# Kernel tuning notes

Hardware: AMD Instinct MI355X
Metric: run time of the kernel (lower is better)

Reference implementation:

```python
import jax, jax.numpy as jnp
import numpy as np

# Sizes: batch, mapper input dim, subspace dim n, ambient dim k (= n, no equalities),
# number of linear inequalities, number of quadratic constraints.
B, IN_DIM, N, K, M_LIN, QC = 32768, 256, 128, 128, 1024, 16


def setup_inputs() -> dict:
    rng = np.random.default_rng(0)
    x = rng.standard_normal((B, IN_DIM, 1), dtype=np.float32)
    # mapper = nn.Linear(IN_DIM, N)
    W = (rng.standard_normal((N, IN_DIM)) / np.sqrt(IN_DIM)).astype(np.float32)
    b = (0.01 * rng.standard_normal((N,))).astype(np.float32)
    # Linear inequalities A_p z <= b_p, strictly feasible at z0 = 0
    z0 = np.zeros((N, 1), dtype=np.float32)
    A_p = rng.standard_normal((M_LIN, N)).astype(np.float32)
    b_p = (A_p @ z0 + rng.uniform(0.5, 1.5, (M_LIN, 1))).astype(np.float32)
    D = (A_p / (b_p - A_p @ z0)).astype(np.float32)  # D = A_p / ((b_p - A_p z0) 1^T)
    # No equality constraints: y = NA_E z + yp with NA_E = I, yp = 0, y0 = z0
    NA_E = np.eye(K, N, dtype=np.float32)
    yp = np.zeros((K, 1), dtype=np.float32)
    y0 = NA_E @ z0 + yp
    # Quadratic constraints 0.5 y'P y + q'y + r <= 0, strictly feasible at y0.
    # Precompute phi, delta exactly as in ConstraintModule.__init__ (RAYEN branch).
    all_phi = np.empty((QC, 1, K), dtype=np.float32)
    all_delta = np.empty((QC, K, K), dtype=np.float32)
    for i in range(QC):
        G = (rng.standard_normal((K, K)) / np.sqrt(K)).astype(np.float32)
        P = G.T @ G + 0.1 * np.eye(K, dtype=np.float32)
        q = (0.1 * rng.standard_normal((K, 1))).astype(np.float32)
        val0 = 0.5 * y0.T @ P @ y0 + q.T @ y0
        r = -(val0 + np.float32(rng.uniform(0.5, 2.0)))  # value at y0 strictly negative
        quad_at_y0 = 0.5 * y0.T @ P @ y0 + q.T @ y0 + r   # [1,1], < 0
        sigma = 2.0 * quad_at_y0                           # scalar < 0
        g = y0.T @ P + q.T                                 # [1,K]
        all_phi[i] = -g / sigma
        all_delta[i] = (g.T @ g - 4.0 * quad_at_y0 * 0.5 * P) / np.square(sigma)
    return {
        "x": jnp.asarray(x),
        "W": jnp.asarray(W),
        "b": jnp.asarray(b),
        "D": jnp.asarray(D),
        "NA_E": jnp.asarray(NA_E),
        "yp": jnp.asarray(yp),
        "z0": jnp.asarray(z0),
        "all_phi": jnp.asarray(all_phi),
        "all_delta": jnp.asarray(all_delta),
    }


def reference(x, W, b, D, NA_E, yp, z0, all_phi, all_delta):
    Bn = x.shape[0]
    # mapper: x.view(B,-1) -> Linear -> unsqueeze(2)
    v = (x.reshape(Bn, -1) @ W.T + b)[:, :, None]                     # [B,n,1]
    norm_v = jnp.sqrt(jnp.sum(v * v, axis=(1, 2), keepdims=True))    # [B,1,1]
    v_bar = v / jnp.maximum(norm_v, 1e-12)                           # F.normalize
    # kappa from linear constraints: relu(max_m (D v_bar)_m)
    Dv = jnp.einsum('mn,bno->bmo', D, v_bar)                         # [B,M,1]
    kappa = jax.nn.relu(jnp.max(Dv, axis=1, keepdims=True))          # [B,1,1]
    # kappa from quadratic constraints: phi_i rho + sqrt(rho' delta_i rho)
    rho = jnp.einsum('kn,bno->bko', NA_E, v_bar)[..., 0]             # [B,k]
    lin_term = rho @ all_phi[:, 0, :].T                              # [B,Q]
    dr = jnp.einsum('qkl,bl->bqk', all_delta, rho)                   # [B,Q,k]
    quad_term = jnp.einsum('bqk,bk->bq', dr, rho)                    # [B,Q]
    kappa_q = lin_term + jnp.sqrt(quad_term)                         # [B,Q]
    kappa_nl = jnp.max(kappa_q, axis=1)[:, None, None]               # [B,1,1]
    kappa = jnp.maximum(kappa, kappa_nl)
    # alpha = min(1/kappa, ||v||); z = z0 + alpha * v_bar; y = NA_E z + yp
    alpha = jnp.minimum(1.0 / kappa, norm_v)
    z = z0 + alpha * v_bar                                           # [B,n,1]
    y = jnp.einsum('kn,bno->bko', NA_E, z) + yp                      # [B,k,1]
    return y
```

## Files before the change

### kernel.cpp

```cpp
#include <hip/hip_runtime.h>
#include <hip/hip_bf16.h>


typedef __attribute__((ext_vector_type(8))) short short8;
typedef __attribute__((ext_vector_type(4))) float f32x4;

__device__ __forceinline__ float bf2f(unsigned short u) {
    union { unsigned int i; float f; } v; v.i = ((unsigned int)u) << 16; return v.f;
}
__device__ __forceinline__ unsigned short f2bf(float f) {
    union { float f; unsigned int i; } v; v.f = f;
    unsigned int r = v.i + 0x7FFFu + ((v.i >> 16) & 1u);
    return (unsigned short)(r >> 16);
}

template<int DT>
__device__ __forceinline__ short8 ld8(const void* p, size_t i) {
    if constexpr (DT == 1) {
        return *reinterpret_cast<const short8*>(reinterpret_cast<const unsigned short*>(p) + i);
    } else {
        const float* f = reinterpret_cast<const float*>(p) + i;
        short8 r;
#pragma unroll
        for (int j = 0; j < 8; ++j) r[j] = (short)f2bf(f[j]);
        return r;
    }
}
template<int DT>
__device__ __forceinline__ float ldf(const void* p, int i) {
    if constexpr (DT == 1) return bf2f(reinterpret_cast<const unsigned short*>(p)[i]);
    else return reinterpret_cast<const float*>(p)[i];
}

__device__ __forceinline__ void glds16(const void* g, void* l) {
    __builtin_amdgcn_global_load_lds(
        (const __attribute__((address_space(1))) void*)g,
        (__attribute__((address_space(3))) void*)l, 16, 0, 0);
}

__global__ void detect_dtype(const unsigned short* __restrict__ x, int* __restrict__ flag) {
    __shared__ int cnt;
    if (threadIdx.x == 0) cnt = 0;
    __syncthreads();
    float a = fabsf(bf2f(x[threadIdx.x]));
    int ok = (a > 1e-3f && a < 1e2f) ? 1 : 0;
    atomicAdd(&cnt, ok);
    __syncthreads();
    if (threadIdx.x == 0) *flag = (cnt > 200) ? 1 : 0;
}

template<int DT, int MODE>
__device__ __forceinline__ void rayen_body(
    const void* xp, const void* Wp, const void* bp, const void* Dp,
    const void* ypp, const void* z0p, const void* phip, const void* dltp,
    void* outp, const int* flag)
{
    if (*flag != DT) return;

    __shared__ unsigned char lds_big[49152];
    __shared__ unsigned char lds_rho[16384];
    __shared__ float lds_nsq[64][4];
    __shared__ float lds_dmax[64][4];
    __shared__ float lds_quad[64][16];
    __shared__ float lds_lin[64][16];
    __shared__ float lds_alpha[64];

    const int tid = threadIdx.x;
    const int lane = tid & 63;
    const int w = tid >> 6;
    const int hi = lane >> 4;
    const int lo = lane & 15;
    const size_t row0 = (size_t)blockIdx.x * 64;

    const unsigned char* Xb = (const unsigned char*)xp;
    const unsigned char* Db = (const unsigned char*)Dp;
    const unsigned char* Qb = (const unsigned char*)dltp;

#pragma unroll
    for (int i = 0; i < 8; ++i) {
        int ch = i * 256 + tid;
        int row = ((ch >> 9) << 4) | (ch & 15);
        int off = (((ch >> 6) & 7) << 6) | (((ch >> 4) & 3) << 4);
        if constexpr (DT == 1)
            glds16(Xb + (row0 + row) * 512 + off, lds_big + ch * 16);
        else {
            short8 v = ld8<0>(Xb, (row0 + row) * 256 + (off >> 1));
            *reinterpret_cast<short8*>(lds_big + ch * 16) = v;
        }
    }

    short8 wf[2][8];
#pragma unroll
    for (int ct = 0; ct < 2; ++ct)
#pragma unroll
        for (int kb = 0; kb < 8; ++kb)
            wf[ct][kb] = ld8<DT>(Wp, (size_t)(w * 32 + ct * 16 + lo) * 256 + kb * 32 + hi * 8);

    asm volatile("s_waitcnt vmcnt(0)" ::: "memory");
    __syncthreads();

    f32x4 acc1[2][4];
#pragma unroll
    for (int c = 0; c < 2; ++c)
#pragma unroll
        for (int r = 0; r < 4; ++r)
#pragma unroll
            for (int e = 0; e < 4; ++e) acc1[c][r][e] = 0.f;

#pragma unroll
    for (int kb = 0; kb < 8; ++kb) {
        short8 af[4];
#pragma unroll
        for (int rt = 0; rt < 4; ++rt)
            af[rt] = *reinterpret_cast<const short8*>(
                lds_big + (((rt << 3) | kb) << 10) + lane * 16);
#pragma unroll
        for (int ct = 0; ct < 2; ++ct)
#pragma unroll
            for (int rt = 0; rt < 4; ++rt)
                acc1[ct][rt] = __builtin_amdgcn_mfma_f32_16x16x32_bf16(af[rt], wf[ct][kb], acc1[ct][rt], 0, 0, 0);
    }

    float bv[2];
#pragma unroll
    for (int ct = 0; ct < 2; ++ct) bv[ct] = ldf<DT>(bp, w * 32 + ct * 16 + lo);
#pragma unroll
    for (int rt = 0; rt < 4; ++rt)
#pragma unroll
        for (int reg = 0; reg < 4; ++reg) {
            float s = 0.f;
#pragma unroll
            for (int ct = 0; ct < 2; ++ct) {
                float v = acc1[ct][rt][reg] + bv[ct];
                acc1[ct][rt][reg] = v;
                s += v * v;
            }
            s += __shfl_xor(s, 1);
            s += __shfl_xor(s, 2);
            s += __shfl_xor(s, 4);
            s += __shfl_xor(s, 8);
            if (lo == 0) lds_nsq[rt * 16 + hi * 4 + reg][w] = s;
        }
    __syncthreads();

#pragma unroll
    for (int rt = 0; rt < 4; ++rt)
#pragma unroll
        for (int reg = 0; reg < 4; ++reg) {
            int row = rt * 16 + hi * 4 + reg;
            float nsq = lds_nsq[row][0] + lds_nsq[row][1] + lds_nsq[row][2] + lds_nsq[row][3];
            float rinv = 1.0f / fmaxf(sqrtf(nsq), 1e-12f);
#pragma unroll
            for (int ct = 0; ct < 2; ++ct) {
                int col = w * 32 + ct * 16 + lo;
                unsigned short u = f2bf(acc1[ct][rt][reg] * rinv);
                *reinterpret_cast<unsigned short*>(
                    lds_rho + row * 256 + ((col * 2) ^ ((row & 7) << 4))) = u;
            }
        }
    __syncthreads();

    short8 af2[4][4];
#pragma unroll
    for (int rt = 0; rt < 4; ++rt)
#pragma unroll
        for (int kb = 0; kb < 4; ++kb) {
            int row = rt * 16 + lo;
            af2[rt][kb] = *reinterpret_cast<const short8*>(
                lds_rho + row * 256 + (((kb << 6) | (hi << 4)) ^ ((lo & 7) << 4)));
        }

    unsigned char* wbase = lds_big + w * 12288;
    auto stage_q = [&](int p, int b) {
        unsigned char* dst0 = wbase + b * 4096;
#pragma unroll
        for (int kb = 0; kb < 4; ++kb) {
            size_t grow;
            const void* base;
            if (p < 16) { base = Dp;   grow = (size_t)(p * 64 + w * 16 + lo); }
            else {
                int pd = p - 16;
                base = dltp;
                grow = (size_t)((((pd >> 3) * 4 + w) * 128) + ((pd & 7) * 16 + lo));
            }
            if constexpr (DT == 1)
                glds16((const unsigned char*)base + grow * 256 + kb * 64 + hi * 16,
                       dst0 + kb * 1024);
            else {
                short8 v = ld8<0>(base, grow * 128 + kb * 32 + hi * 8);
                *reinterpret_cast<short8*>(dst0 + kb * 1024 + lane * 16) = v;
            }
        }
    };

    f32x4 dmax[4];
#pragma unroll
    for (int rt = 0; rt < 4; ++rt)
#pragma unroll
        for (int e = 0; e < 4; ++e) dmax[rt][e] = -3e38f;
    f32x4 qsum[4];
#pragma unroll
    for (int rt = 0; rt < 4; ++rt)
#pragma unroll
        for (int e = 0; e < 4; ++e) qsum[rt][e] = 0.f;

    if constexpr (MODE != 1) {
        stage_q(0, 0);
        stage_q(1, 1);
#pragma unroll 1
        for (int p = 0; p < 48; ++p) {
            if constexpr (DT == 1) {
                if (p < 47) { asm volatile("s_waitcnt vmcnt(4)" ::: "memory"); }
                else        { asm volatile("s_waitcnt vmcnt(0)" ::: "memory"); }
            } else {
                asm volatile("s_waitcnt vmcnt(0) lgkmcnt(0)" ::: "memory");
            }
            __builtin_amdgcn_sched_barrier(0);
            if (p + 2 < 48) stage_q(p + 2, (p + 2) % 3);

            if constexpr (MODE != 2) {
                unsigned char* buf = wbase + (p % 3) * 4096;
                f32x4 acc[4];
#pragma unroll
                for (int rt = 0; rt < 4; ++rt)
#pragma unroll
                    for (int e = 0; e < 4; ++e) acc[rt][e] = 0.f;
#pragma unroll
                for (int kb = 0; kb < 4; ++kb) {
                    short8 bf = *reinterpret_cast<const short8*>(buf + kb * 1024 + lane * 16);
#pragma unroll
                    for (int rt = 0; rt < 4; ++rt)
                        acc[rt] = __builtin_amdgcn_mfma_f32_16x16x32_bf16(af2[rt][kb], bf, acc[rt], 0, 0, 0);
                }

                if (MODE == 3 || p < 16) {
#pragma unroll
                    for (int rt = 0; rt < 4; ++rt)
#pragma unroll
                        for (int e = 0; e < 4; ++e) dmax[rt][e] = fmaxf(dmax[rt][e], acc[rt][e]);
                } else {
                    int pd = p - 16;
                    int kr = (pd & 7) << 4;
#pragma unroll
                    for (int rt = 0; rt < 4; ++rt)
#pragma unroll
                        for (int e = 0; e < 4; ++e) {
                            int row = rt * 16 + hi * 4 + e;
                            float rvv = bf2f(*reinterpret_cast<const unsigned short*>(
                                lds_rho + row * 256 + ((((kr + lo) * 2)) ^ ((row & 7) << 4))));
                            qsum[rt][e] += acc[rt][e] * rvv;
                        }
                    if ((pd & 7) == 7) {
#pragma unroll
                        for (int rt = 0; rt < 4; ++rt)
#pragma unroll
                            for (int e = 0; e < 4; ++e) {
                                float s = qsum[rt][e];
                                s += __shfl_xor(s, 1);
                                s += __shfl_xor(s, 2);
                                s += __shfl_xor(s, 4);
                                s += __shfl_xor(s, 8);
                                if (lo == 0) lds_quad[rt * 16 + hi * 4 + e][((pd >> 3) << 2) | w] = s;
                                qsum[rt][e] = 0.f;
                            }
                    }
                }
            }
        }
    }

    if constexpr (MODE == 0 || MODE == 3) {
#pragma unroll
        for (int rt = 0; rt < 4; ++rt)
#pragma unroll
            for (int reg = 0; reg < 4; ++reg) {
                float m = dmax[rt][reg];
                m = fmaxf(m, __shfl_xor(m, 1));
                m = fmaxf(m, __shfl_xor(m, 2));
                m = fmaxf(m, __shfl_xor(m, 4));
                m = fmaxf(m, __shfl_xor(m, 8));
                if (lo == 0) lds_dmax[rt * 16 + hi * 4 + reg][w] = m;
            }
    }
    if constexpr (MODE == 1 || MODE == 2) {
        if (tid < 64) {
#pragma unroll
            for (int j = 0; j < 4; ++j) lds_dmax[tid][j] = 0.f;
        }
    }
    if constexpr (MODE != 0) {
        if (tid < 64) {
#pragma unroll
            for (int q = 0; q < 16; ++q) lds_quad[tid][q] = 0.f;
        }
    }

    if (w == 0) {
        f32x4 accp[4];
#pragma unroll
        for (int rt = 0; rt < 4; ++rt)
#pragma unroll
            for (int e = 0; e < 4; ++e) accp[rt][e] = 0.f;
#pragma unroll
        for (int kb = 0; kb < 4; ++kb) {
            short8 bp8 = ld8<DT>(phip, (size_t)lo * 128 + kb * 32 + hi * 8);
#pragma unroll
            for (int rt = 0; rt < 4; ++rt)
                accp[rt] = __builtin_amdgcn_mfma_f32_16x16x32_bf16(af2[rt][kb], bp8, accp[rt], 0, 0, 0);
        }
#pragma unroll
        for (int rt = 0; rt < 4; ++rt)
#pragma unroll
            for (int reg = 0; reg < 4; ++reg)
                lds_lin[rt * 16 + hi * 4 + reg][lo] = accp[rt][reg];
    }
    __syncthreads();

    if (tid < 64) {
        int row = tid;
        float nsq = lds_nsq[row][0] + lds_nsq[row][1] + lds_nsq[row][2] + lds_nsq[row][3];
        float norm = sqrtf(nsq);
        float kap = fmaxf(0.f, fmaxf(fmaxf(lds_dmax[row][0], lds_dmax[row][1]),
                                     fmaxf(lds_dmax[row][2], lds_dmax[row][3])));
#pragma unroll
        for (int q = 0; q < 16; ++q) {
            float kq = lds_lin[row][q] + sqrtf(fmaxf(lds_quad[row][q], 0.f));
            kap = fmaxf(kap, kq);
        }
        lds_alpha[row] = fminf(1.0f / kap, norm);
    }
    __syncthreads();

#pragma unroll
    for (int i = 0; i < 4; ++i) {
        int idx = tid + i * 256;
        int row = idx >> 4;
        int col0 = (idx & 15) * 8;
        float alpha = lds_alpha[row];
        short8 r8 = *reinterpret_cast<const short8*>(
            lds_rho + row * 256 + ((col0 * 2) ^ ((row & 7) << 4)));
        float yv[8];
#pragma unroll
        for (int j = 0; j < 8; ++j) {
            float vb = bf2f((unsigned short)r8[j]);
            yv[j] = ldf<DT>(z0p, col0 + j) + alpha * vb + ldf<DT>(ypp, col0 + j);
        }
        size_t obase = (row0 + row) * 128 + col0;
        if constexpr (DT == 1) {
            short8 pack;
#pragma unroll
            for (int j = 0; j < 8; ++j) pack[j] = (short)f2bf(yv[j]);
            *reinterpret_cast<short8*>(reinterpret_cast<unsigned short*>(outp) + obase) = pack;
        } else {
            f32x4 p0, p1;
#pragma unroll
            for (int j = 0; j < 4; ++j) { p0[j] = yv[j]; p1[j] = yv[4 + j]; }
            *reinterpret_cast<f32x4*>(reinterpret_cast<float*>(outp) + obase) = p0;
            *reinterpret_cast<f32x4*>(reinterpret_cast<float*>(outp) + obase + 4) = p1;
        }
    }
}

#define ARGS const void* xp, const void* Wp, const void* bp, const void* Dp, \
             const void* ypp, const void* z0p, const void* phip, const void* dltp, \
             void* outp, const int* flag
#define PASS xp, Wp, bp, Dp, ypp, z0p, phip, dltp, outp, flag

template<int DT>
__global__ __launch_bounds__(256, 2) void rayen_full(ARGS)      { rayen_body<DT, 0>(PASS); }
__global__ __launch_bounds__(256, 2) void rayen_abl_nopanel(ARGS)   { rayen_body<1, 1>(PASS); }
__global__ __launch_bounds__(256, 2) void rayen_abl_stageonly(ARGS) { rayen_body<1, 2>(PASS); }
__global__ __launch_bounds__(256, 2) void rayen_abl_mfmaonly(ARGS)  { rayen_body<1, 3>(PASS); }

extern "C" void kernel_launch(void* const* d_in, const int* in_sizes, int n_in,
                              void* d_out, int out_size, void* d_ws, size_t ws_size,
                              hipStream_t stream) {
    const void* x    = d_in[0];
    const void* W    = d_in[1];
    const void* b    = d_in[2];
    const void* D    = d_in[3];
    const void* yp   = d_in[5];
    const void* z0   = d_in[6];
    const void* phi  = d_in[7];
    const void* dlt  = d_in[8];
    int* flag = reinterpret_cast<int*>(d_ws);

    const int B = in_sizes[0] / 256;
    dim3 grid(B / 64), blk(256);

    detect_dtype<<<dim3(1), dim3(256), 0, stream>>>(
        reinterpret_cast<const unsigned short*>(x), flag);
    rayen_abl_nopanel<<<grid, blk, 0, stream>>>(x, W, b, D, yp, z0, phi, dlt, d_out, flag);
    rayen_abl_stageonly<<<grid, blk, 0, stream>>>(x, W, b, D, yp, z0, phi, dlt, d_out, flag);
    rayen_abl_mfmaonly<<<grid, blk, 0, stream>>>(x, W, b, D, yp, z0, phi, dlt, d_out, flag);
    rayen_full<1><<<grid, blk, 0, stream>>>(x, W, b, D, yp, z0, phi, dlt, d_out, flag);
    rayen_full<0><<<grid, blk, 0, stream>>>(x, W, b, D, yp, z0, phi, dlt, d_out, flag);
}
```

Baseline: 127.7 us.

## Split fused RAYEN kernel into staged kernels and drop ablation launches

Replaces the monolithic per-tile kernel with four kernels: a mapper GEMM that writes normalized v_bar and norms to workspace, a linear-constraint max kernel split over 4 M-groups, a quadratic-constraint kernel split over 16 constraints, and a small output kernel. It also stops launching the three ablation kernels that previously ran alongside the full kernel on every call. The goal is more blocks per stage for better occupancy, no serial 48-step panel loop per tile, and no redundant work. In exchange, v_bar makes an extra round trip through global memory, it re-stages from workspace, and more kernels are launched. It falls back to the fused kernel when the workspace is too small.

```diff
diff --git a/kernel.cpp b/kernel.cpp
--- a/kernel.cpp
+++ b/kernel.cpp
@@ -49,14 +49,340 @@
     if (threadIdx.x == 0) *flag = (cnt > 200) ? 1 : 0;
 }
 
-template<int DT, int MODE>
-__device__ __forceinline__ void rayen_body(
+template<int DT>
+__global__ __launch_bounds__(256, 2) void k1_vbar(
+    const void* __restrict__ xp, const void* __restrict__ Wp, const void* __restrict__ bp,
+    unsigned short* __restrict__ rho_g, float* __restrict__ norm_g,
+    const int* __restrict__ flag)
+{
+    if (*flag != DT) return;
+    __shared__ unsigned char lds_x[32768];
+    __shared__ unsigned char lds_v[16384];
+    __shared__ float lds_nsq[64][4];
+
+    const int tid = threadIdx.x;
+    const int lane = tid & 63;
+    const int w = tid >> 6, hi = lane >> 4, lo = lane & 15;
+    const size_t row0 = (size_t)blockIdx.x * 64;
+    const unsigned char* Xb = (const unsigned char*)xp;
+
+#pragma unroll
+    for (int i = 0; i < 8; ++i) {
+        int ch = i * 256 + tid;
+        int row = ((ch >> 9) << 4) | (ch & 15);
+        int off = (((ch >> 6) & 7) << 6) | (((ch >> 4) & 3) << 4);
+        if constexpr (DT == 1)
+            glds16(Xb + (row0 + row) * 512 + off, lds_x + ch * 16);
+        else {
+            short8 v = ld8<0>(Xb, (row0 + row) * 256 + (off >> 1));
+            *reinterpret_cast<short8*>(lds_x + ch * 16) = v;
+        }
+    }
+    short8 wf[2][8];
+#pragma unroll
+    for (int ct = 0; ct < 2; ++ct)
+#pragma unroll
+        for (int kb = 0; kb < 8; ++kb)
+            wf[ct][kb] = ld8<DT>(Wp, (size_t)(w * 32 + ct * 16 + lo) * 256 + kb * 32 + hi * 8);
+    asm volatile("s_waitcnt vmcnt(0)" ::: "memory");
+    __syncthreads();
+
+    f32x4 acc1[2][4];
+#pragma unroll
+    for (int c = 0; c < 2; ++c)
+#pragma unroll
+        for (int r = 0; r < 4; ++r)
+#pragma unroll
+            for (int e = 0; e < 4; ++e) acc1[c][r][e] = 0.f;
+#pragma unroll
+    for (int kb = 0; kb < 8; ++kb) {
+        short8 af[4];
+#pragma unroll
+        for (int rt = 0; rt < 4; ++rt)
+            af[rt] = *reinterpret_cast<const short8*>(lds_x + (((rt << 3) | kb) << 10) + lane * 16);
+#pragma unroll
+        for (int ct = 0; ct < 2; ++ct)
+#pragma unroll
+            for (int rt = 0; rt < 4; ++rt)
+                acc1[ct][rt] = __builtin_amdgcn_mfma_f32_16x16x32_bf16(af[rt], wf[ct][kb], acc1[ct][rt], 0, 0, 0);
+    }
+    float bv[2];
+#pragma unroll
+    for (int ct = 0; ct < 2; ++ct) bv[ct] = ldf<DT>(bp, w * 32 + ct * 16 + lo);
+#pragma unroll
+    for (int rt = 0; rt < 4; ++rt)
+#pragma unroll
+        for (int reg = 0; reg < 4; ++reg) {
+            float s = 0.f;
+#pragma unroll
+            for (int ct = 0; ct < 2; ++ct) {
+                float v = acc1[ct][rt][reg] + bv[ct];
+                acc1[ct][rt][reg] = v;
+                s += v * v;
+            }
+            s += __shfl_xor(s, 1); s += __shfl_xor(s, 2);
+            s += __shfl_xor(s, 4); s += __shfl_xor(s, 8);
+            if (lo == 0) lds_nsq[rt * 16 + hi * 4 + reg][w] = s;
+        }
+    __syncthreads();
+
+#pragma unroll
+    for (int rt = 0; rt < 4; ++rt)
+#pragma unroll
+        for (int reg = 0; reg < 4; ++reg) {
+            int row = rt * 16 + hi * 4 + reg;
+            float nsq = lds_nsq[row][0] + lds_nsq[row][1] + lds_nsq[row][2] + lds_nsq[row][3];
+            float rinv = 1.0f / fmaxf(sqrtf(nsq), 1e-12f);
+#pragma unroll
+            for (int ct = 0; ct < 2; ++ct) {
+                int col = w * 32 + ct * 16 + lo;
+                *reinterpret_cast<unsigned short*>(lds_v + row * 256 + col * 2) =
+                    f2bf(acc1[ct][rt][reg] * rinv);
+            }
+        }
+    if (tid < 64) {
+        float nsq = lds_nsq[tid][0] + lds_nsq[tid][1] + lds_nsq[tid][2] + lds_nsq[tid][3];
+        norm_g[row0 + tid] = sqrtf(nsq);
+    }
+    __syncthreads();
+#pragma unroll
+    for (int i = 0; i < 4; ++i) {
+        int ch = i * 256 + tid;
+        int row = ch >> 4, c16 = ch & 15;
+        *reinterpret_cast<short8*>(rho_g + (row0 + row) * 128 + c16 * 8) =
+            *reinterpret_cast<const short8*>(lds_v + row * 256 + c16 * 16);
+    }
+}
+
+__device__ __forceinline__ void stage_rho(const unsigned short* rho_g, size_t row0,
+                                          unsigned char* lds_rho, int tid) {
+#pragma unroll
+    for (int i = 0; i < 4; ++i) {
+        int ch = i * 256 + tid;
+        int row = ch >> 4;
+        int off = (ch & 15) * 16;
+        glds16((const unsigned char*)rho_g + (row0 + row) * 256 + (off ^ ((row & 7) << 4)),
+               lds_rho + ch * 16);
+    }
+}
+
+template<int DT>
+__global__ __launch_bounds__(256, 2) void k2a_dmax(
+    const void* __restrict__ Dp, const unsigned short* __restrict__ rho_g,
+    float* __restrict__ dmax_g, const int* __restrict__ flag)
+{
+    if (*flag != DT) return;
+    __shared__ unsigned char lds_rho[16384];
+    __shared__ float lds_red[64][4];
+    const int tid = threadIdx.x;
+    const int lane = tid & 63;
+    const int w = tid >> 6, hi = lane >> 4, lo = lane & 15;
+    const size_t row0 = (size_t)blockIdx.x * 64;
+    const int mg = blockIdx.y;
+
+    stage_rho(rho_g, row0, lds_rho, tid);
+    asm volatile("s_waitcnt vmcnt(0)" ::: "memory");
+    __syncthreads();
+
+    short8 af2[4][4];
+#pragma unroll
+    for (int rt = 0; rt < 4; ++rt)
+#pragma unroll
+        for (int kb = 0; kb < 4; ++kb) {
+            int row = rt * 16 + lo;
+            af2[rt][kb] = *reinterpret_cast<const short8*>(
+                lds_rho + row * 256 + (((kb << 6) | (hi << 4)) ^ ((lo & 7) << 4)));
+        }
+
+    f32x4 dmax[4];
+#pragma unroll
+    for (int rt = 0; rt < 4; ++rt)
+#pragma unroll
+        for (int e = 0; e < 4; ++e) dmax[rt][e] = -3e38f;
+
+#pragma unroll
+    for (int t = 0; t < 4; ++t) {
+        int col = mg * 256 + w * 64 + t * 16 + lo;
+        short8 bD[4];
+#pragma unroll
+        for (int kb = 0; kb < 4; ++kb)
+            bD[kb] = ld8<DT>(Dp, (size_t)col * 128 + kb * 32 + hi * 8);
+        f32x4 acc[4];
+#pragma unroll
+        for (int rt = 0; rt < 4; ++rt)
+#pragma unroll
+            for (int e = 0; e < 4; ++e) acc[rt][e] = 0.f;
+#pragma unroll
+        for (int kb = 0; kb < 4; ++kb)
+#pragma unroll
+            for (int rt = 0; rt < 4; ++rt)
+                acc[rt] = __builtin_amdgcn_mfma_f32_16x16x32_bf16(af2[rt][kb], bD[kb], acc[rt], 0, 0, 0);
+#pragma unroll
+        for (int rt = 0; rt < 4; ++rt)
+#pragma unroll
+            for (int e = 0; e < 4; ++e) dmax[rt][e] = fmaxf(dmax[rt][e], acc[rt][e]);
+    }
+#pragma unroll
+    for (int rt = 0; rt < 4; ++rt)
+#pragma unroll
+        for (int reg = 0; reg < 4; ++reg) {
+            float m = dmax[rt][reg];
+            m = fmaxf(m, __shfl_xor(m, 1)); m = fmaxf(m, __shfl_xor(m, 2));
+            m = fmaxf(m, __shfl_xor(m, 4)); m = fmaxf(m, __shfl_xor(m, 8));
+            if (lo == 0) lds_red[rt * 16 + hi * 4 + reg][w] = m;
+        }
+    __syncthreads();
+    if (tid < 64) {
+        float m = fmaxf(fmaxf(lds_red[tid][0], lds_red[tid][1]),
+                        fmaxf(lds_red[tid][2], lds_red[tid][3]));
+        dmax_g[(row0 + tid) * 4 + mg] = m;
+    }
+}
+
+template<int DT>
+__global__ __launch_bounds__(256, 2) void k2b_quad(
+    const void* __restrict__ dltp, const void* __restrict__ phip,
+    const unsigned short* __restrict__ rho_g,
+    float* __restrict__ kq_g, const int* __restrict__ flag)
+{
+    if (*flag != DT) return;
+    __shared__ unsigned char lds_rho[16384];
+    __shared__ float lds_q[64][4];
+    __shared__ float lds_l[64][4];
+    const int tid = threadIdx.x;
+    const int lane = tid & 63;
+    const int w = tid >> 6, hi = lane >> 4, lo = lane & 15;
+    const size_t row0 = (size_t)blockIdx.x * 64;
+    const int q = blockIdx.y;
+
+    stage_rho(rho_g, row0, lds_rho, tid);
+    asm volatile("s_waitcnt vmcnt(0)" ::: "memory");
+    __syncthreads();
+
+    short8 af2[4][4];
+#pragma unroll
+    for (int rt = 0; rt < 4; ++rt)
+#pragma unroll
+        for (int kb = 0; kb < 4; ++kb) {
+            int row = rt * 16 + lo;
+            af2[rt][kb] = *reinterpret_cast<const short8*>(
+                lds_rho + row * 256 + (((kb << 6) | (hi << 4)) ^ ((lo & 7) << 4)));
+        }
+
+    f32x4 qsum[4], lsum[4];
+#pragma unroll
+    for (int rt = 0; rt < 4; ++rt)
+#pragma unroll
+        for (int e = 0; e < 4; ++e) { qsum[rt][e] = 0.f; lsum[rt][e] = 0.f; }
+
+#pragma unroll
+    for (int t = 0; t < 2; ++t) {
+        int colk = w * 32 + t * 16 + lo;
+        short8 bq[4];
+#pragma unroll
+        for (int kb = 0; kb < 4; ++kb)
+            bq[kb] = ld8<DT>(dltp, ((size_t)q * 128 + colk) * 128 + kb * 32 + hi * 8);
+        float phv = ldf<DT>(phip, q * 128 + colk);
+        f32x4 acc[4];
+#pragma unroll
+        for (int rt = 0; rt < 4; ++rt)
+#pragma unroll
+            for (int e = 0; e < 4; ++e) acc[rt][e] = 0.f;
+#pragma unroll
+        for (int kb = 0; kb < 4; ++kb)
+#pragma unroll
+            for (int rt = 0; rt < 4; ++rt)
+                acc[rt] = __builtin_amdgcn_mfma_f32_16x16x32_bf16(af2[rt][kb], bq[kb], acc[rt], 0, 0, 0);
+#pragma unroll
+        for (int rt = 0; rt < 4; ++rt)
+#pragma unroll
+            for (int e = 0; e < 4; ++e) {
+                int row = rt * 16 + hi * 4 + e;
+                float rv = bf2f(*reinterpret_cast<const unsigned short*>(
+                    lds_rho + row * 256 + ((colk * 2) ^ ((row & 7) << 4))));
+                qsum[rt][e] += acc[rt][e] * rv;
+                lsum[rt][e] += rv * phv;
+            }
+    }
+#pragma unroll
+    for (int rt = 0; rt < 4; ++rt)
+#pragma unroll
+        for (int reg = 0; reg < 4; ++reg) {
+            float s = qsum[rt][reg];
+            s += __shfl_xor(s, 1); s += __shfl_xor(s, 2);
+            s += __shfl_xor(s, 4); s += __shfl_xor(s, 8);
+            float l = lsum[rt][reg];
+            l += __shfl_xor(l, 1); l += __shfl_xor(l, 2);
+            l += __shfl_xor(l, 4); l += __shfl_xor(l, 8);
+            if (lo == 0) {
+                lds_q[rt * 16 + hi * 4 + reg][w] = s;
+                lds_l[rt * 16 + hi * 4 + reg][w] = l;
+            }
+        }
+    __syncthreads();
+    if (tid < 64) {
+        float quad = lds_q[tid][0] + lds_q[tid][1] + lds_q[tid][2] + lds_q[tid][3];
+        float lin  = lds_l[tid][0] + lds_l[tid][1] + lds_l[tid][2] + lds_l[tid][3];
+        kq_g[(row0 + tid) * 16 + q] = lin + sqrtf(fmaxf(quad, 0.f));
+    }
+}
+
+template<int DT>
+__global__ __launch_bounds__(256, 2) void k3_out(
+    const unsigned short* __restrict__ rho_g, const float* __restrict__ norm_g,
+    const float* __restrict__ dmax_g, const float* __restrict__ kq_g,
+    const void* __restrict__ z0p, const void* __restrict__ ypp,
+    void* __restrict__ outp, const int* __restrict__ flag)
+{
+    if (*flag != DT) return;
+    __shared__ float lds_alpha[64];
+    const int tid = threadIdx.x;
+    const size_t row0 = (size_t)blockIdx.x * 64;
+
+    if (tid < 64) {
+        size_t rg = row0 + tid;
+        float kap = 0.f;
+#pragma unroll
+        for (int mg = 0; mg < 4; ++mg) kap = fmaxf(kap, dmax_g[rg * 4 + mg]);
+#pragma unroll
+        for (int qq = 0; qq < 16; ++qq) kap = fmaxf(kap, kq_g[rg * 16 + qq]);
+        lds_alpha[tid] = fminf(1.0f / kap, norm_g[rg]);
+    }
+    __syncthreads();
+#pragma unroll
+    for (int i = 0; i < 4; ++i) {
+        int idx = tid + i * 256;
+        int row = idx >> 4;
+        int col0 = (idx & 15) * 8;
+        float alpha = lds_alpha[row];
+        short8 r8 = *reinterpret_cast<const short8*>(rho_g + (row0 + row) * 128 + col0);
+        float yv[8];
+#pragma unroll
+        for (int j = 0; j < 8; ++j)
+            yv[j] = ldf<DT>(z0p, col0 + j) + alpha * bf2f((unsigned short)r8[j]) + ldf<DT>(ypp, col0 + j);
+        size_t obase = (row0 + row) * 128 + col0;
+        if constexpr (DT == 1) {
+            short8 pack;
+#pragma unroll
+            for (int j = 0; j < 8; ++j) pack[j] = (short)f2bf(yv[j]);
+            *reinterpret_cast<short8*>(reinterpret_cast<unsigned short*>(outp) + obase) = pack;
+        } else {
+            f32x4 p0, p1;
+#pragma unroll
+            for (int j = 0; j < 4; ++j) { p0[j] = yv[j]; p1[j] = yv[4 + j]; }
+            *reinterpret_cast<f32x4*>(reinterpret_cast<float*>(outp) + obase) = p0;
+            *reinterpret_cast<f32x4*>(reinterpret_cast<float*>(outp) + obase + 4) = p1;
+        }
+    }
+}
+
+template<int DT>
+__global__ __launch_bounds__(256, 2) void rayen_mono(
     const void* xp, const void* Wp, const void* bp, const void* Dp,
     const void* ypp, const void* z0p, const void* phip, const void* dltp,
     void* outp, const int* flag)
 {
     if (*flag != DT) return;
-
     __shared__ unsigned char lds_big[49152];
     __shared__ unsigned char lds_rho[16384];
     __shared__ float lds_nsq[64][4];
@@ -67,14 +393,9 @@
 
     const int tid = threadIdx.x;
     const int lane = tid & 63;
-    const int w = tid >> 6;
-    const int hi = lane >> 4;
-    const int lo = lane & 15;
+    const int w = tid >> 6, hi = lane >> 4, lo = lane & 15;
     const size_t row0 = (size_t)blockIdx.x * 64;
-
     const unsigned char* Xb = (const unsigned char*)xp;
-    const unsigned char* Db = (const unsigned char*)Dp;
-    const unsigned char* Qb = (const unsigned char*)dltp;
 
 #pragma unroll
     for (int i = 0; i < 8; ++i) {
@@ -88,14 +409,12 @@
             *reinterpret_cast<short8*>(lds_big + ch * 16) = v;
         }
     }
-
     short8 wf[2][8];
 #pragma unroll
     for (int ct = 0; ct < 2; ++ct)
 #pragma unroll
         for (int kb = 0; kb < 8; ++kb)
             wf[ct][kb] = ld8<DT>(Wp, (size_t)(w * 32 + ct * 16 + lo) * 256 + kb * 32 + hi * 8);
-
     asm volatile("s_waitcnt vmcnt(0)" ::: "memory");
     __syncthreads();
 
@@ -106,21 +425,18 @@
         for (int r = 0; r < 4; ++r)
 #pragma unroll
             for (int e = 0; e < 4; ++e) acc1[c][r][e] = 0.f;
-
 #pragma unroll
     for (int kb = 0; kb < 8; ++kb) {
         short8 af[4];
 #pragma unroll
         for (int rt = 0; rt < 4; ++rt)
-            af[rt] = *reinterpret_cast<const short8*>(
-                lds_big + (((rt << 3) | kb) << 10) + lane * 16);
+            af[rt] = *reinterpret_cast<const short8*>(lds_big + (((rt << 3) | kb) << 10) + lane * 16);
 #pragma unroll
         for (int ct = 0; ct < 2; ++ct)
 #pragma unroll
             for (int rt = 0; rt < 4; ++rt)
                 acc1[ct][rt] = __builtin_amdgcn_mfma_f32_16x16x32_bf16(af[rt], wf[ct][kb], acc1[ct][rt], 0, 0, 0);
     }
-
     float bv[2];
 #pragma unroll
     for (int ct = 0; ct < 2; ++ct) bv[ct] = ldf<DT>(bp, w * 32 + ct * 16 + lo);
@@ -135,14 +451,11 @@
                 acc1[ct][rt][reg] = v;
                 s += v * v;
             }
-            s += __shfl_xor(s, 1);
-            s += __shfl_xor(s, 2);
-            s += __shfl_xor(s, 4);
-            s += __shfl_xor(s, 8);
+            s += __shfl_xor(s, 1); s += __shfl_xor(s, 2);
+            s += __shfl_xor(s, 4); s += __shfl_xor(s, 8);
             if (lo == 0) lds_nsq[rt * 16 + hi * 4 + reg][w] = s;
         }
     __syncthreads();
-
 #pragma unroll
     for (int rt = 0; rt < 4; ++rt)
 #pragma unroll
@@ -153,13 +466,12 @@
 #pragma unroll
             for (int ct = 0; ct < 2; ++ct) {
                 int col = w * 32 + ct * 16 + lo;
-                unsigned short u = f2bf(acc1[ct][rt][reg] * rinv);
                 *reinterpret_cast<unsigned short*>(
-                    lds_rho + row * 256 + ((col * 2) ^ ((row & 7) << 4))) = u;
-            }
-        }
-    __syncthreads();
-
+                    lds_rho + row * 256 + ((col * 2) ^ ((row & 7) << 4))) =
+                    f2bf(acc1[ct][rt][reg] * rinv);
+            }
+        }
+    __syncthreads();
     short8 af2[4][4];
 #pragma unroll
     for (int rt = 0; rt < 4; ++rt)
@@ -169,132 +481,94 @@
             af2[rt][kb] = *reinterpret_cast<const short8*>(
                 lds_rho + row * 256 + (((kb << 6) | (hi << 4)) ^ ((lo & 7) << 4)));
         }
-
     unsigned char* wbase = lds_big + w * 12288;
     auto stage_q = [&](int p, int b) {
         unsigned char* dst0 = wbase + b * 4096;
 #pragma unroll
         for (int kb = 0; kb < 4; ++kb) {
-            size_t grow;
-            const void* base;
-            if (p < 16) { base = Dp;   grow = (size_t)(p * 64 + w * 16 + lo); }
+            size_t grow; const void* base;
+            if (p < 16) { base = Dp; grow = (size_t)(p * 64 + w * 16 + lo); }
             else {
                 int pd = p - 16;
                 base = dltp;
                 grow = (size_t)((((pd >> 3) * 4 + w) * 128) + ((pd & 7) * 16 + lo));
             }
             if constexpr (DT == 1)
-                glds16((const unsigned char*)base + grow * 256 + kb * 64 + hi * 16,
-                       dst0 + kb * 1024);
+                glds16((const unsigned char*)base + grow * 256 + kb * 64 + hi * 16, dst0 + kb * 1024);
             else {
                 short8 v = ld8<0>(base, grow * 128 + kb * 32 + hi * 8);
                 *reinterpret_cast<short8*>(dst0 + kb * 1024 + lane * 16) = v;
             }
         }
     };
-
-    f32x4 dmax[4];
-#pragma unroll
-    for (int rt = 0; rt < 4; ++rt)
-#pragma unroll
-        for (int e = 0; e < 4; ++e) dmax[rt][e] = -3e38f;
-    f32x4 qsum[4];
-#pragma unroll
-    for (int rt = 0; rt < 4; ++rt)
-#pragma unroll
-        for (int e = 0; e < 4; ++e) qsum[rt][e] = 0.f;
-
-    if constexpr (MODE != 1) {
-        stage_q(0, 0);
-        stage_q(1, 1);
+    f32x4 dmax[4], qsum[4];
+#pragma unroll
+    for (int rt = 0; rt < 4; ++rt)
+#pragma unroll
+        for (int e = 0; e < 4; ++e) { dmax[rt][e] = -3e38f; qsum[rt][e] = 0.f; }
+    stage_q(0, 0); stage_q(1, 1);
 #pragma unroll 1
-        for (int p = 0; p < 48; ++p) {
-            if constexpr (DT == 1) {
-                if (p < 47) { asm volatile("s_waitcnt vmcnt(4)" ::: "memory"); }
-                else        { asm volatile("s_waitcnt vmcnt(0)" ::: "memory"); }
-            } else {
-                asm volatile("s_waitcnt vmcnt(0) lgkmcnt(0)" ::: "memory");
-            }
-            __builtin_amdgcn_sched_barrier(0);
-            if (p + 2 < 48) stage_q(p + 2, (p + 2) % 3);
-
-            if constexpr (MODE != 2) {
-                unsigned char* buf = wbase + (p % 3) * 4096;
-                f32x4 acc[4];
+    for (int p = 0; p < 48; ++p) {
+        if constexpr (DT == 1) {
+            if (p < 47) { asm volatile("s_waitcnt vmcnt(4)" ::: "memory"); }
+            else        { asm volatile("s_waitcnt vmcnt(0)" ::: "memory"); }
+        } else {
+            asm volatile("s_waitcnt vmcnt(0) lgkmcnt(0)" ::: "memory");
+        }
+        __builtin_amdgcn_sched_barrier(0);
+        if (p + 2 < 48) stage_q(p + 2, (p + 2) % 3);
+        unsigned char* buf = wbase + (p % 3) * 4096;
+        f32x4 acc[4];
+#pragma unroll
+        for (int rt = 0; rt < 4; ++rt)
+#pragma unroll
+            for (int e = 0; e < 4; ++e) acc[rt][e] = 0.f;
+#pragma unroll
+        for (int kb = 0; kb < 4; ++kb) {
+            short8 bf = *reinterpret_cast<const short8*>(buf + kb * 1024 + lane * 16);
+#pragma unroll
+            for (int rt = 0; rt < 4; ++rt)
+                acc[rt] = __builtin_amdgcn_mfma_f32_16x16x32_bf16(af2[rt][kb], bf, acc[rt], 0, 0, 0);
+        }
+        if (p < 16) {
+#pragma unroll
+            for (int rt = 0; rt < 4; ++rt)
+#pragma unroll
+                for (int e = 0; e < 4; ++e) dmax[rt][e] = fmaxf(dmax[rt][e], acc[rt][e]);
+        } else {
+            int pd = p - 16, kr = (pd & 7) << 4;
+#pragma unroll
+            for (int rt = 0; rt < 4; ++rt)
+#pragma unroll
+                for (int e = 0; e < 4; ++e) {
+                    int row = rt * 16 + hi * 4 + e;
+                    float rvv = bf2f(*reinterpret_cast<const unsigned short*>(
+                        lds_rho + row * 256 + ((((kr + lo) * 2)) ^ ((row & 7) << 4))));
+                    qsum[rt][e] += acc[rt][e] * rvv;
+                }
+            if ((pd & 7) == 7) {
 #pragma unroll
                 for (int rt = 0; rt < 4; ++rt)
 #pragma unroll
-                    for (int e = 0; e < 4; ++e) acc[rt][e] = 0.f;
-#pragma unroll
-                for (int kb = 0; kb < 4; ++kb) {
-                    short8 bf = *reinterpret_cast<const short8*>(buf + kb * 1024 + lane * 16);
-#pragma unroll
-                    for (int rt = 0; rt < 4; ++rt)
-                        acc[rt] = __builtin_amdgcn_mfma_f32_16x16x32_bf16(af2[rt][kb], bf, acc[rt], 0, 0, 0);
-                }
-
-                if (MODE == 3 || p < 16) {
-#pragma unroll
-                    for (int rt = 0; rt < 4; ++rt)
-#pragma unroll
-                        for (int e = 0; e < 4; ++e) dmax[rt][e] = fmaxf(dmax[rt][e], acc[rt][e]);
-                } else {
-                    int pd = p - 16;
-                    int kr = (pd & 7) << 4;
-#pragma unroll
-                    for (int rt = 0; rt < 4; ++rt)
-#pragma unroll
-                        for (int e = 0; e < 4; ++e) {
-                            int row = rt * 16 + hi * 4 + e;
-                            float rvv = bf2f(*reinterpret_cast<const unsigned short*>(
-                                lds_rho + row * 256 + ((((kr + lo) * 2)) ^ ((row & 7) << 4))));
-                            qsum[rt][e] += acc[rt][e] * rvv;
-                        }
-                    if ((pd & 7) == 7) {
-#pragma unroll
-                        for (int rt = 0; rt < 4; ++rt)
-#pragma unroll
-                            for (int e = 0; e < 4; ++e) {
-                                float s = qsum[rt][e];
-                                s += __shfl_xor(s, 1);
-                                s += __shfl_xor(s, 2);
-                                s += __shfl_xor(s, 4);
-                                s += __shfl_xor(s, 8);
-                                if (lo == 0) lds_quad[rt * 16 + hi * 4 + e][((pd >> 3) << 2) | w] = s;
-                                qsum[rt][e] = 0.f;
-                            }
+                    for (int e = 0; e < 4; ++e) {
+                        float s = qsum[rt][e];
+                        s += __shfl_xor(s, 1); s += __shfl_xor(s, 2);
+                        s += __shfl_xor(s, 4); s += __shfl_xor(s, 8);
+                        if (lo == 0) lds_quad[rt * 16 + hi * 4 + e][((pd >> 3) << 2) | w] = s;
+                        qsum[rt][e] = 0.f;
                     }
-                }
-            }
-        }
-    }
-
-    if constexpr (MODE == 0 || MODE == 3) {
-#pragma unroll
-        for (int rt = 0; rt < 4; ++rt)
-#pragma unroll
-            for (int reg = 0; reg < 4; ++reg) {
-                float m = dmax[rt][reg];
-                m = fmaxf(m, __shfl_xor(m, 1));
-                m = fmaxf(m, __shfl_xor(m, 2));
-                m = fmaxf(m, __shfl_xor(m, 4));
-                m = fmaxf(m, __shfl_xor(m, 8));
-                if (lo == 0) lds_dmax[rt * 16 + hi * 4 + reg][w] = m;
-            }
-    }
-    if constexpr (MODE == 1 || MODE == 2) {
-        if (tid < 64) {
-#pragma unroll
-            for (int j = 0; j < 4; ++j) lds_dmax[tid][j] = 0.f;
-        }
-    }
-    if constexpr (MODE != 0) {
-        if (tid < 64) {
-#pragma unroll
-            for (int q = 0; q < 16; ++q) lds_quad[tid][q] = 0.f;
-        }
-    }
-
+            }
+        }
+    }
+#pragma unroll
+    for (int rt = 0; rt < 4; ++rt)
+#pragma unroll
+        for (int reg = 0; reg < 4; ++reg) {
+            float m = dmax[rt][reg];
+            m = fmaxf(m, __shfl_xor(m, 1)); m = fmaxf(m, __shfl_xor(m, 2));
+            m = fmaxf(m, __shfl_xor(m, 4)); m = fmaxf(m, __shfl_xor(m, 8));
+            if (lo == 0) lds_dmax[rt * 16 + hi * 4 + reg][w] = m;
+        }
     if (w == 0) {
         f32x4 accp[4];
 #pragma unroll
@@ -315,7 +589,6 @@
                 lds_lin[rt * 16 + hi * 4 + reg][lo] = accp[rt][reg];
     }
     __syncthreads();
-
     if (tid < 64) {
         int row = tid;
         float nsq = lds_nsq[row][0] + lds_nsq[row][1] + lds_nsq[row][2] + lds_nsq[row][3];
@@ -323,28 +596,22 @@
         float kap = fmaxf(0.f, fmaxf(fmaxf(lds_dmax[row][0], lds_dmax[row][1]),
                                      fmaxf(lds_dmax[row][2], lds_dmax[row][3])));
 #pragma unroll
-        for (int q = 0; q < 16; ++q) {
-            float kq = lds_lin[row][q] + sqrtf(fmaxf(lds_quad[row][q], 0.f));
-            kap = fmaxf(kap, kq);
-        }
+        for (int q = 0; q < 16; ++q)
+            kap = fmaxf(kap, lds_lin[row][q] + sqrtf(fmaxf(lds_quad[row][q], 0.f)));
         lds_alpha[row] = fminf(1.0f / kap, norm);
     }
     __syncthreads();
-
 #pragma unroll
     for (int i = 0; i < 4; ++i) {
         int idx = tid + i * 256;
-        int row = idx >> 4;
-        int col0 = (idx & 15) * 8;
+        int row = idx >> 4, col0 = (idx & 15) * 8;
         float alpha = lds_alpha[row];
         short8 r8 = *reinterpret_cast<const short8*>(
             lds_rho + row * 256 + ((col0 * 2) ^ ((row & 7) << 4)));
         float yv[8];
 #pragma unroll
-        for (int j = 0; j < 8; ++j) {
-            float vb = bf2f((unsigned short)r8[j]);
-            yv[j] = ldf<DT>(z0p, col0 + j) + alpha * vb + ldf<DT>(ypp, col0 + j);
-        }
+        for (int j = 0; j < 8; ++j)
+            yv[j] = ldf<DT>(z0p, col0 + j) + alpha * bf2f((unsigned short)r8[j]) + ldf<DT>(ypp, col0 + j);
         size_t obase = (row0 + row) * 128 + col0;
         if constexpr (DT == 1) {
             short8 pack;
@@ -360,17 +627,6 @@
         }
     }
 }
-
-#define ARGS const void* xp, const void* Wp, const void* bp, const void* Dp, \
-             const void* ypp, const void* z0p, const void* phip, const void* dltp, \
-             void* outp, const int* flag
-#define PASS xp, Wp, bp, Dp, ypp, z0p, phip, dltp, outp, flag
-
-template<int DT>
-__global__ __launch_bounds__(256, 2) void rayen_full(ARGS)      { rayen_body<DT, 0>(PASS); }
-__global__ __launch_bounds__(256, 2) void rayen_abl_nopanel(ARGS)   { rayen_body<1, 1>(PASS); }
-__global__ __launch_bounds__(256, 2) void rayen_abl_stageonly(ARGS) { rayen_body<1, 2>(PASS); }
-__global__ __launch_bounds__(256, 2) void rayen_abl_mfmaonly(ARGS)  { rayen_body<1, 3>(PASS); }
 
 extern "C" void kernel_launch(void* const* d_in, const int* in_sizes, int n_in,
                               void* d_out, int out_size, void* d_ws, size_t ws_size,
@@ -383,16 +639,34 @@
     const void* z0   = d_in[6];
     const void* phi  = d_in[7];
     const void* dlt  = d_in[8];
-    int* flag = reinterpret_cast<int*>(d_ws);
 
     const int B = in_sizes[0] / 256;
-    dim3 grid(B / 64), blk(256);
+    const int tiles = B / 64;
+
+    unsigned char* ws = reinterpret_cast<unsigned char*>(d_ws);
+    int* flag = reinterpret_cast<int*>(ws);
+    unsigned short* rho_g = reinterpret_cast<unsigned short*>(ws + 4096);
+    float* norm_g = reinterpret_cast<float*>(ws + 4096 + (size_t)B * 256);
+    float* dmax_g = reinterpret_cast<float*>(ws + 4096 + (size_t)B * 256 + (size_t)B * 4);
+    float* kq_g   = reinterpret_cast<float*>(ws + 4096 + (size_t)B * 256 + (size_t)B * 4 + (size_t)B * 16);
+    const size_t need = 4096 + (size_t)B * 256 + (size_t)B * 4 + (size_t)B * 16 + (size_t)B * 64;
 
     detect_dtype<<<dim3(1), dim3(256), 0, stream>>>(
         reinterpret_cast<const unsigned short*>(x), flag);
-    rayen_abl_nopanel<<<grid, blk, 0, stream>>>(x, W, b, D, yp, z0, phi, dlt, d_out, flag);
-    rayen_abl_stageonly<<<grid, blk, 0, stream>>>(x, W, b, D, yp, z0, phi, dlt, d_out, flag);
-    rayen_abl_mfmaonly<<<grid, blk, 0, stream>>>(x, W, b, D, yp, z0, phi, dlt, d_out, flag);
-    rayen_full<1><<<grid, blk, 0, stream>>>(x, W, b, D, yp, z0, phi, dlt, d_out, flag);
-    rayen_full<0><<<grid, blk, 0, stream>>>(x, W, b, D, yp, z0, phi, dlt, d_out, flag);
-}
+
+    if (ws_size >= need) {
+        dim3 blk(256);
+        k1_vbar<1><<<dim3(tiles), blk, 0, stream>>>(x, W, b, rho_g, norm_g, flag);
+        k1_vbar<0><<<dim3(tiles), blk, 0, stream>>>(x, W, b, rho_g, norm_g, flag);
+        k2a_dmax<1><<<dim3(tiles, 4), blk, 0, stream>>>(D, rho_g, dmax_g, flag);
+        k2a_dmax<0><<<dim3(tiles, 4), blk, 0, stream>>>(D, rho_g, dmax_g, flag);
+        k2b_quad<1><<<dim3(tiles, 16), blk, 0, stream>>>(dlt, phi, rho_g, kq_g, flag);
+        k2b_quad<0><<<dim3(tiles, 16), blk, 0, stream>>>(dlt, phi, rho_g, kq_g, flag);
+        k3_out<1><<<dim3(tiles), blk, 0, stream>>>(rho_g, norm_g, dmax_g, kq_g, z0, yp, d_out, flag);
+        k3_out<0><<<dim3(tiles), blk, 0, stream>>>(rho_g, norm_g, dmax_g, kq_g, z0, yp, d_out, flag);
+    } else {
+        dim3 blk(256);
+        rayen_mono<1><<<dim3(tiles), blk, 0, stream>>>(x, W, b, D, yp, z0, phi, dlt, d_out, flag);
+        rayen_mono<0><<<dim3(tiles), blk, 0, stream>>>(x, W, b, D, yp, z0, phi, dlt, d_out, flag);
+    }
+}
```

New measurement: 155.3 us. +21.6%, slower.
